# Kernel optimization log

Hardware: AMD Instinct MI355X
Metric: run time of the kernel (lower is better)

Reference implementation:

```python
import jax, jax.numpy as jnp
import numpy as np

B, D, DEPTH, C = 8192, 2048, 10, 1000
NUM_INNER = 2 ** DEPTH - 1   # 1023
NUM_LEAVES = 2 ** DEPTH      # 1024


def setup_inputs() -> dict:
    key = jax.random.key(0)
    k1, k2, k3, k4 = jax.random.split(key, 4)
    x = jax.random.normal(k1, (B, D), dtype=jnp.float32)
    # scale weights like a typical init so sigmoid isn't fully saturated
    W = jax.random.normal(k2, (D, NUM_INNER), dtype=jnp.float32) * 0.02
    b = jax.random.normal(k3, (NUM_INNER,), dtype=jnp.float32) * 0.02
    leaf_dist = jax.random.normal(k4, (NUM_LEAVES, C), dtype=jnp.float32)
    return {"x": x, "W": W, "b": b, "leaf_dist": leaf_dist}


def reference(x, W, b, leaf_dist):
    # inner node routing probabilities: [B, num_inner]
    decisions = jax.nn.sigmoid(x @ W + b)
    depth = int(np.log2(decisions.shape[1] + 1))
    pp = jnp.ones((x.shape[0], 1), dtype=x.dtype)  # path probs, starts at root
    for d in range(depth):  # small fixed loop over tree depth
        s, e = 2 ** d - 1, 2 ** (d + 1) - 1
        ld = decisions[:, s:e]                      # [B, 2^d]
        pp = jnp.concatenate([pp * ld, pp * (1.0 - ld)], axis=1)  # [B, 2^(d+1)]
        # faithful reproduction of the original's even/odd reordering
        pp = jnp.concatenate([pp[:, ::2], pp[:, 1::2]], axis=1)
    leaf_probs = jax.nn.softmax(leaf_dist, axis=1)  # [num_leaves, C]
    return pp @ leaf_probs                          # [B, C]
```

## Files before the change

kernel.cpp:

```cpp
#include <hip/hip_runtime.h>

typedef __attribute__((ext_vector_type(8))) unsigned short ushort8v;
typedef __attribute__((ext_vector_type(8))) __bf16 bf16x8;
typedef __attribute__((ext_vector_type(4))) float floatx4;

__device__ __forceinline__ unsigned short f2b(float f) {
    unsigned u = __float_as_uint(f);
    unsigned r = u + 0x7fffu + ((u >> 16) & 1u);
    return (unsigned short)(r >> 16);
}
__device__ __forceinline__ float b2f(unsigned short h) {
    return __uint_as_float(((unsigned)h) << 16);
}

__device__ __forceinline__ void gload16(const void* g, void* l) {
    __builtin_amdgcn_global_load_lds(
        (const __attribute__((address_space(1))) unsigned int*)g,
        (__attribute__((address_space(3))) unsigned int*)l,
        16, 0, 0);
}


__global__ __launch_bounds__(256) void prep_kernel(const float* __restrict__ x,
                                                   unsigned short* __restrict__ A2x,
                                                   const float* __restrict__ W,
                                                   unsigned short* __restrict__ B2w,
                                                   const float* __restrict__ ld_,
                                                   unsigned short* __restrict__ B2p) {
    __shared__ float tile[32 * 33];
    __shared__ float buf[1000];
    __shared__ float red[8];
    const int b = blockIdx.x, t = threadIdx.x;
    if (b < 2048) {
        const int mt = b >> 2, kq = (b & 3) * 64;
        const int kco = t >> 4, l16 = t & 15;
        const float* xr0 = x + (size_t)(mt * 16 + l16) * 2048;
#pragma unroll
        for (int i = 0; i < 4; i++) {
            const int kc = kq + i * 16 + kco;
            const float* xr = xr0 + kc * 8;
            float4 v0 = *(const float4*)xr;
            float4 v1 = *(const float4*)(xr + 4);
            ushort8v o;
            o[0] = f2b(v0.x); o[1] = f2b(v0.y); o[2] = f2b(v0.z); o[3] = f2b(v0.w);
            o[4] = f2b(v1.x); o[5] = f2b(v1.y); o[6] = f2b(v1.z); o[7] = f2b(v1.w);
            *(ushort8v*)(A2x + ((size_t)(mt * 256 + kc) * 16 + l16) * 8) = o;
        }
    } else if (b < 4096) {
        const int idx = b - 2048;
        const int n0 = (idx & 31) * 32, k0 = (idx >> 5) * 32;
        const int tx = t & 31, ty = t >> 5;
#pragma unroll
        for (int i = 0; i < 4; i++) {
            int k = k0 + ty + i * 8, n = n0 + tx;
            tile[(ty + i * 8) * 33 + tx] = (n < 1023) ? W[(size_t)k * 1023 + n] : 0.f;
        }
        __syncthreads();
#pragma unroll
        for (int i = 0; i < 4; i++) {
            int n = n0 + ty + i * 8, k = k0 + tx;
            size_t off = ((size_t)((n >> 4) * 256 + (k >> 3)) * 16 + (n & 15)) * 8 + (k & 7);
            B2w[off] = f2b(tile[tx * 33 + ty + i * 8]);
        }
    } else {
        const int l0 = b - 4096;
        const float* r = ld_ + (size_t)l0 * 1000;
        float mx = -3.4e38f;
        for (int i = t; i < 1000; i += 256) { float v = r[i]; buf[i] = v; mx = fmaxf(mx, v); }
#pragma unroll
        for (int o = 32; o > 0; o >>= 1) mx = fmaxf(mx, __shfl_down(mx, o));
        if ((t & 63) == 0) red[t >> 6] = mx;
        __syncthreads();
        mx = fmaxf(fmaxf(red[0], red[1]), fmaxf(red[2], red[3]));
        float s = 0.f;
        for (int i = t; i < 1000; i += 256) { float e = __expf(buf[i] - mx); buf[i] = e; s += e; }
#pragma unroll
        for (int o = 32; o > 0; o >>= 1) s += __shfl_down(s, o);
        if ((t & 63) == 0) red[4 + (t >> 6)] = s;
        __syncthreads();
        float inv = 1.f / (red[4] + red[5] + red[6] + red[7]);
        for (int i = t; i < 1024; i += 256) {
            float pv = (i < 1000) ? buf[i] * inv : 0.f;
            size_t off = ((size_t)((i >> 4) * 128 + (l0 >> 3)) * 16 + (i & 15)) * 8 + (l0 & 7);
            B2p[off] = f2b(pv);
        }
    }
}

__global__ __launch_bounds__(256) void pp_kernel(const unsigned short* __restrict__ dec,
                                                 unsigned short* __restrict__ A2p) {
    __shared__ unsigned short dsh[8 * 1024];
    __shared__ float pa[8 * 1024];
    __shared__ float pb[8 * 1024];
    const int t = threadIdx.x;
    const int r0 = blockIdx.x * 8;
    {
        const ushort8v* src = (const ushort8v*)(dec + (size_t)r0 * 1024);
        ushort8v* dst = (ushort8v*)dsh;
        for (int g = t; g < 1024; g += 256) dst[g] = src[g];
    }
    if (t < 8) pa[t * 1024] = 1.f;
    __syncthreads();
    float* cur = pa; float* nxt = pb;
    for (int dep = 0; dep < 10; dep++) {
        const int half = 1 << dep;
        const int len  = half << 1;
        const int total = len << 3;
        for (int idx = t; idx < total; idx += 256) {
            const int r = idx >> (dep + 1);
            const int j = idx & (len - 1);
            int tt = j >> dep;
            int s  = j & (half - 1);
            int i2 = 2 * s + tt;
            int u  = i2 >> dep;
            int rr = i2 & (half - 1);
            float dv = b2f(dsh[r * 1024 + half - 1 + rr]);
            nxt[r * 1024 + j] = cur[r * 1024 + rr] * (u ? (1.f - dv) : dv);
        }
        __syncthreads();
        float* tmp = cur; cur = nxt; nxt = tmp;
    }
    for (int i = t; i < 8192; i += 256) {
        const int r = i >> 10, j = i & 1023;
        const int rrow = r0 + r;
        size_t off = ((size_t)((rrow >> 4) * 128 + (j >> 3)) * 16 + (rrow & 15)) * 8 + (j & 7);
        A2p[off] = f2b(cur[r * 1024 + j]);
    }
}

#define VMW(N) asm volatile("s_waitcnt vmcnt(" #N ")" ::: "memory")

#define M1_STEP(ks_, CUR_, STG_, VM_, DOSTAGE_)                                       \
    {                                                                                 \
        if (DOSTAGE_) STAGE((ks_) + 2, (STG_));                                       \
        VMW(VM_);                                                                     \
        __builtin_amdgcn_s_barrier();                                                 \
        const unsigned short* lA = &lds[(CUR_)][0];                                   \
        const unsigned short* lB = &lds[(CUR_)][8192];                                \
        bf16x8 af[4], bv[4];                                                          \
        _Pragma("unroll")                                                             \
        for (int m2 = 0; m2 < 4; m2++)                                                \
            af[m2] = __builtin_bit_cast(bf16x8,                                       \
                *(const ushort8v*)&lA[((wr * 4 + m2) * 4 + quad) * 128 + l16 * 8]);   \
        _Pragma("unroll")                                                             \
        for (int n2 = 0; n2 < 4; n2++)                                                \
            bv[n2] = __builtin_bit_cast(bf16x8,                                       \
                *(const ushort8v*)&lB[((wc * 4 + n2) * 4 + quad) * 128 + l16 * 8]);   \
        asm volatile("s_waitcnt lgkmcnt(0)" ::: "memory");                            \
        __builtin_amdgcn_sched_barrier(0);                                            \
        __builtin_amdgcn_s_setprio(1);                                                \
        _Pragma("unroll")                                                             \
        for (int m2 = 0; m2 < 4; m2++)                                                \
            _Pragma("unroll")                                                         \
            for (int n2 = 0; n2 < 4; n2++)                                            \
                acc[m2][n2] = __builtin_amdgcn_mfma_f32_16x16x32_bf16(                \
                    af[m2], bv[n2], acc[m2][n2], 0, 0, 0);                            \
        __builtin_amdgcn_s_setprio(0);                                                \
        __builtin_amdgcn_s_barrier();                                                 \
    }

__global__ __launch_bounds__(512, 1) void gemm_m1(const unsigned short* __restrict__ A2,
                                                  const unsigned short* __restrict__ B2,
                                                  const float* __restrict__ bias,
                                                  unsigned short* __restrict__ obf) {
    constexpr int KC = 256;
    __shared__ unsigned short lds[3][12288];

    const int tid  = threadIdx.x;
    const int lane = tid & 63;
    const int wave = tid >> 6;
    const int quad = lane >> 4, l16 = lane & 15;
    const int wr = wave >> 1, wc = wave & 1;

    const int bid = blockIdx.x;
    const int xcd = bid & 7;
    const int j   = bid >> 3;
    const int bm  = xcd * 4 + (j & 3);
    const int bn  = j >> 2;

    const int cA  = tid >> 4;
    const int sub = (tid & 15) * 8;
    const unsigned short* gA0 = A2 + ((size_t)(bm * 16 + (cA >> 2))        * KC + (cA & 3)) * 128 + sub;
    const unsigned short* gA1 = A2 + ((size_t)(bm * 16 + ((cA + 32) >> 2)) * KC + (cA & 3)) * 128 + sub;
    const unsigned short* gB0 = B2 + ((size_t)(bn * 8  + (cA >> 2))        * KC + (cA & 3)) * 128 + sub;
    const int dA0 = cA * 128 + sub;
    const int dA1 = (cA + 32) * 128 + sub;
    const int dB0 = 8192 + cA * 128 + sub;

    floatx4 acc[4][4] = {};
    constexpr int nks = KC / 4;

    auto STAGE = [&](int ks, int b) {
        const size_t ko = (size_t)ks * 512;
        gload16(gA0 + ko, &lds[b][dA0]);
        gload16(gA1 + ko, &lds[b][dA1]);
        gload16(gB0 + ko, &lds[b][dB0]);
    };

    STAGE(0, 0); STAGE(1, 1);

    int c0 = 0, c1 = 1, c2 = 2;
    for (int ks = 0; ks < nks - 2; ++ks) {
        M1_STEP(ks, c0, c2, 6, true);
        int tmp = c0; c0 = c1; c1 = c2; c2 = tmp;
    }
    M1_STEP(nks - 2, c0, c2, 3, false);
    { int tmp = c0; c0 = c1; c1 = c2; c2 = tmp; }
    M1_STEP(nks - 1, c0, c2, 0, false);

    const int mt0 = bm * 16 + wr * 4;
    const int nt0 = bn * 8  + wc * 4;
#pragma unroll
    for (int n2 = 0; n2 < 4; n2++) {
        const int col = (nt0 + n2) * 16 + l16;
        const float bbias = (col < 1023) ? bias[col] : 0.f;
#pragma unroll
        for (int m2 = 0; m2 < 4; m2++) {
            const int row0 = (mt0 + m2) * 16 + quad * 4;
#pragma unroll
            for (int r = 0; r < 4; r++) {
                float sgm = 1.f / (1.f + __expf(-(acc[m2][n2][r] + bbias)));
                obf[(size_t)(row0 + r) * 1024 + col] = f2b(sgm);
            }
        }
    }
}

#define P4_STEP(ks_, b_, VM_, DOSTAGE_)                                             \
    {                                                                               \
        VMW(VM_);                                                                   \
        __builtin_amdgcn_s_barrier();                                               \
        __builtin_amdgcn_sched_barrier(0);                                          \
        const unsigned short* lA = &lds[(b_)][0];                                   \
        const unsigned short* lB = &lds[(b_)][4096];                                \
        bf16x8 af[4], bv[4];                                                        \
        _Pragma("unroll")                                                           \
        for (int m2 = 0; m2 < 4; m2++)                                              \
            af[m2] = __builtin_bit_cast(bf16x8,                                     \
                *(const ushort8v*)&lA[((wr * 4 + m2) * 4 + quad) * 128 + l16 * 8]); \
        _Pragma("unroll")                                                           \
        for (int n2 = 0; n2 < 4; n2++)                                              \
            bv[n2] = __builtin_bit_cast(bf16x8,                                     \
                *(const ushort8v*)&lB[((wc * 4 + n2) * 4 + quad) * 128 + l16 * 8]); \
        asm volatile("s_waitcnt lgkmcnt(0)" ::: "memory");                          \
        __builtin_amdgcn_sched_barrier(0);                                          \
        __builtin_amdgcn_s_barrier();                                               \
        __builtin_amdgcn_sched_barrier(0);                                          \
        if (DOSTAGE_) STAGE((ks_) + 4, (b_));                                       \
        __builtin_amdgcn_s_setprio(1);                                              \
        _Pragma("unroll")                                                           \
        for (int m2 = 0; m2 < 4; m2++)                                              \
            _Pragma("unroll")                                                       \
            for (int n2 = 0; n2 < 4; n2++)                                          \
                acc[m2][n2] = __builtin_amdgcn_mfma_f32_16x16x32_bf16(              \
                    af[m2], bv[n2], acc[m2][n2], 0, 0, 0);                          \
        __builtin_amdgcn_s_setprio(0);                                              \
    }

template <int KC>
__global__ __launch_bounds__(256, 2) void gemm_p4(const unsigned short* __restrict__ A2,
                                                  const unsigned short* __restrict__ B2,
                                                  float* __restrict__ of32, int ldo) {
    __shared__ unsigned short lds[4][8192];

    const int tid  = threadIdx.x;
    const int lane = tid & 63;
    const int wave = tid >> 6;
    const int quad = lane >> 4, l16 = lane & 15;
    const int wr = wave >> 1, wc = wave & 1;

    const int bid = blockIdx.x;
    const int xcd = bid & 7;
    const int j   = bid >> 3;
    const int bm  = xcd * 8 + (j & 7);
    const int bn  = j >> 3;

    const int c0  = tid >> 4;
    const int sub = (tid & 15) * 8;
    const unsigned short* gA0 = A2 + ((size_t)(bm * 8 + (c0 >> 2))        * KC + (c0 & 3)) * 128 + sub;
    const unsigned short* gA1 = A2 + ((size_t)(bm * 8 + ((c0 + 16) >> 2)) * KC + (c0 & 3)) * 128 + sub;
    const unsigned short* gB0 = B2 + ((size_t)(bn * 8 + (c0 >> 2))        * KC + (c0 & 3)) * 128 + sub;
    const unsigned short* gB1 = B2 + ((size_t)(bn * 8 + ((c0 + 16) >> 2)) * KC + (c0 & 3)) * 128 + sub;
    const int dA0 = c0 * 128 + sub;
    const int dA1 = (c0 + 16) * 128 + sub;
    const int dB0 = 4096 + c0 * 128 + sub;
    const int dB1 = 4096 + (c0 + 16) * 128 + sub;

    floatx4 acc[4][4] = {};
    constexpr int nks = KC / 4;

    auto STAGE = [&](int ks, int b) {
        const size_t ko = (size_t)ks * 512;
        gload16(gA0 + ko, &lds[b][dA0]);
        gload16(gA1 + ko, &lds[b][dA1]);
        gload16(gB0 + ko, &lds[b][dB0]);
        gload16(gB1 + ko, &lds[b][dB1]);
    };

    STAGE(0, 0); STAGE(1, 1); STAGE(2, 2); STAGE(3, 3);

    for (int ks = 0; ks < nks - 4; ++ks) {
        P4_STEP(ks, ks & 3, 12, true);
    }
    P4_STEP(nks - 4, (nks - 4) & 3, 12, false);
    P4_STEP(nks - 3, (nks - 3) & 3, 8,  false);
    P4_STEP(nks - 2, (nks - 2) & 3, 4,  false);
    P4_STEP(nks - 1, (nks - 1) & 3, 0,  false);

    const int mt0 = bm * 8 + wr * 4;
    const int nt0 = bn * 8 + wc * 4;
#pragma unroll
    for (int n2 = 0; n2 < 4; n2++) {
        const int col = (nt0 + n2) * 16 + l16;
#pragma unroll
        for (int m2 = 0; m2 < 4; m2++) {
            const int row0 = (mt0 + m2) * 16 + quad * 4;
#pragma unroll
            for (int r = 0; r < 4; r++) {
                if (col < 1000) of32[(size_t)(row0 + r) * ldo + col] = acc[m2][n2][r];
            }
        }
    }
}

extern "C" void kernel_launch(void* const* d_in, const int* in_sizes, int n_in,
                              void* d_out, int out_size, void* d_ws, size_t ws_size,
                              hipStream_t stream) {
    const float* x   = (const float*)d_in[0];
    const float* W   = (const float*)d_in[1];
    const float* b   = (const float*)d_in[2];
    const float* ldd = (const float*)d_in[3];
    float* out = (float*)d_out;

    char* ws = (char*)d_ws;
    unsigned short* A2x = (unsigned short*)(ws);
    unsigned short* A2p = (unsigned short*)(ws);
    unsigned short* B2w = (unsigned short*)(ws + 33554432);
    unsigned short* dec = (unsigned short*)(ws + 37748736);
    unsigned short* B2p = (unsigned short*)(ws + 54525952);

    prep_kernel<<<5120, 256, 0, stream>>>(x, A2x, W, B2w, ldd, B2p);
    gemm_m1<<<256, 512, 0, stream>>>(A2x, B2w, b, dec);
    pp_kernel<<<1024, 256, 0, stream>>>(dec, A2p);
    gemm_p4<128><<<512, 256, 0, stream>>>(A2p, B2p, out, 1000);
}
```

Baseline: 199.8 us.

## Vectorize prep/pp stores and compute first six tree levels directly

The x-conversion path now has each thread read a contiguous run of one row, and the W transpose writes 4 bf16 values per store instead of scalar stores. In pp_kernel, the first six tree levels are computed in closed form per leaf, as a product of six factors, instead of six barrier-separated passes. The iterative loop now starts at depth 6. The final A2p writeout uses 8-byte vector stores, cutting the count of scalar global stores and barriers at the cost of slightly more per-thread index math.

```diff
diff --git a/kernel.cpp b/kernel.cpp
--- a/kernel.cpp
+++ b/kernel.cpp
@@ -1,6 +1,7 @@
 #include <hip/hip_runtime.h>
 
 typedef __attribute__((ext_vector_type(8))) unsigned short ushort8v;
+typedef __attribute__((ext_vector_type(4))) unsigned short ushort4v;
 typedef __attribute__((ext_vector_type(8))) __bf16 bf16x8;
 typedef __attribute__((ext_vector_type(4))) float floatx4;
 
@@ -33,17 +34,17 @@
     const int b = blockIdx.x, t = threadIdx.x;
     if (b < 2048) {
         const int mt = b >> 2, kq = (b & 3) * 64;
-        const int kco = t >> 4, l16 = t & 15;
-        const float* xr0 = x + (size_t)(mt * 16 + l16) * 2048;
-#pragma unroll
-        for (int i = 0; i < 4; i++) {
-            const int kc = kq + i * 16 + kco;
-            const float* xr = xr0 + kc * 8;
-            float4 v0 = *(const float4*)xr;
-            float4 v1 = *(const float4*)(xr + 4);
+        const int l16 = t >> 4;
+        const int sg  = t & 15;
+        const float* xr = x + (size_t)(mt * 16 + l16) * 2048 + (size_t)(kq + sg * 4) * 8;
+#pragma unroll
+        for (int c = 0; c < 4; c++) {
+            float4 v0 = *(const float4*)(xr + c * 8);
+            float4 v1 = *(const float4*)(xr + c * 8 + 4);
             ushort8v o;
             o[0] = f2b(v0.x); o[1] = f2b(v0.y); o[2] = f2b(v0.z); o[3] = f2b(v0.w);
             o[4] = f2b(v1.x); o[5] = f2b(v1.y); o[6] = f2b(v1.z); o[7] = f2b(v1.w);
+            const int kc = kq + sg * 4 + c;
             *(ushort8v*)(A2x + ((size_t)(mt * 256 + kc) * 16 + l16) * 8) = o;
         }
     } else if (b < 4096) {
@@ -56,11 +57,15 @@
             tile[(ty + i * 8) * 33 + tx] = (n < 1023) ? W[(size_t)k * 1023 + n] : 0.f;
         }
         __syncthreads();
-#pragma unroll
-        for (int i = 0; i < 4; i++) {
-            int n = n0 + ty + i * 8, k = k0 + tx;
+        {
+            const int tx2 = t & 31, ky = t >> 5;
+            const int n = n0 + tx2;
+            const int k = k0 + ky * 4;
+            ushort4v o;
+#pragma unroll
+            for (int e = 0; e < 4; e++) o[e] = f2b(tile[(ky * 4 + e) * 33 + tx2]);
             size_t off = ((size_t)((n >> 4) * 256 + (k >> 3)) * 16 + (n & 15)) * 8 + (k & 7);
-            B2w[off] = f2b(tile[tx * 33 + ty + i * 8]);
+            *(ushort4v*)(B2w + off) = o;
         }
     } else {
         const int l0 = b - 4096;
@@ -99,10 +104,36 @@
         ushort8v* dst = (ushort8v*)dsh;
         for (int g = t; g < 1024; g += 256) dst[g] = src[g];
     }
-    if (t < 8) pa[t * 1024] = 1.f;
+    __syncthreads();
+    {
+        const int r  = t >> 5;
+        const int jb = (t & 31) * 2;
+        const unsigned short* dr = &dsh[r * 1024];
+#pragma unroll
+        for (int e = 0; e < 2; e++) {
+            int idx = jb + e;
+            float fac[6];
+#pragma unroll
+            for (int dep = 5; dep >= 0; --dep) {
+                const int half = 1 << dep;
+                const int tt = idx >> dep;
+                const int s  = idx & (half - 1);
+                const int i2 = 2 * s + tt;
+                const int u  = i2 >> dep;
+                const int rr = i2 & (half - 1);
+                const float dv = b2f(dr[half - 1 + rr]);
+                fac[dep] = u ? (1.f - dv) : dv;
+                idx = rr;
+            }
+            float prod = fac[0];
+#pragma unroll
+            for (int dep = 1; dep < 6; dep++) prod *= fac[dep];
+            pa[r * 1024 + jb + e] = prod;
+        }
+    }
     __syncthreads();
     float* cur = pa; float* nxt = pb;
-    for (int dep = 0; dep < 10; dep++) {
+    for (int dep = 6; dep < 10; dep++) {
         const int half = 1 << dep;
         const int len  = half << 1;
         const int total = len << 3;
@@ -120,11 +151,21 @@
         __syncthreads();
         float* tmp = cur; cur = nxt; nxt = tmp;
     }
-    for (int i = t; i < 8192; i += 256) {
-        const int r = i >> 10, j = i & 1023;
+    {
+        const int r  = t >> 5;
+        const int jb = (t & 31) * 32;
         const int rrow = r0 + r;
-        size_t off = ((size_t)((rrow >> 4) * 128 + (j >> 3)) * 16 + (rrow & 15)) * 8 + (j & 7);
-        A2p[off] = f2b(cur[r * 1024 + j]);
+        const float* cr = &cur[r * 1024];
+        const size_t rbase = (size_t)(rrow >> 4) * 128 * 128 + (size_t)(rrow & 15) * 8;
+#pragma unroll
+        for (int g = 0; g < 8; g++) {
+            const int j = jb + g * 4;
+            ushort4v o;
+            o[0] = f2b(cr[j]); o[1] = f2b(cr[j + 1]);
+            o[2] = f2b(cr[j + 2]); o[3] = f2b(cr[j + 3]);
+            size_t off = rbase + (size_t)(j >> 3) * 128 + (j & 7);
+            *(ushort4v*)(A2p + off) = o;
+        }
     }
 }
 
```

Result: no change. 198.7 us (-0.5%).

## Fuse prep, both GEMMs and path-prob stage into one cooperative persistent kernel

Applied to the files above, without the earlier changes.

Replaces the four separate launches (prep, decision GEMM, path-probability, output GEMM) with a single cooperative kernel of 256 blocks × 512 threads, separated by grid-wide syncs. The path-probability stage now computes each leaf's probability directly as a product of ten ancestor factors per thread, instead of level-by-level passes with block barriers. The W transpose also writes 4-wide vector stores. The aim is to remove inter-kernel launch gaps and the barrier-heavy tree expansion. The costs are grid.sync overhead, fixed one-block-per-CU occupancy, and redundant factor recomputation per leaf.

```diff
diff --git a/kernel.cpp b/kernel.cpp
--- a/kernel.cpp
+++ b/kernel.cpp
@@ -1,6 +1,10 @@
 #include <hip/hip_runtime.h>
+#include <hip/hip_cooperative_groups.h>
+
+namespace cg = cooperative_groups;
 
 typedef __attribute__((ext_vector_type(8))) unsigned short ushort8v;
+typedef __attribute__((ext_vector_type(4))) unsigned short ushort4v;
 typedef __attribute__((ext_vector_type(8))) __bf16 bf16x8;
 typedef __attribute__((ext_vector_type(4))) float floatx4;
 
@@ -12,7 +16,6 @@
 __device__ __forceinline__ float b2f(unsigned short h) {
     return __uint_as_float(((unsigned)h) << 16);
 }
-
 __device__ __forceinline__ void gload16(const void* g, void* l) {
     __builtin_amdgcn_global_load_lds(
         (const __attribute__((address_space(1))) unsigned int*)g,
@@ -20,123 +23,16 @@
         16, 0, 0);
 }
 
-
-__global__ __launch_bounds__(256) void prep_kernel(const float* __restrict__ x,
-                                                   unsigned short* __restrict__ A2x,
-                                                   const float* __restrict__ W,
-                                                   unsigned short* __restrict__ B2w,
-                                                   const float* __restrict__ ld_,
-                                                   unsigned short* __restrict__ B2p) {
-    __shared__ float tile[32 * 33];
-    __shared__ float buf[1000];
-    __shared__ float red[8];
-    const int b = blockIdx.x, t = threadIdx.x;
-    if (b < 2048) {
-        const int mt = b >> 2, kq = (b & 3) * 64;
-        const int kco = t >> 4, l16 = t & 15;
-        const float* xr0 = x + (size_t)(mt * 16 + l16) * 2048;
-#pragma unroll
-        for (int i = 0; i < 4; i++) {
-            const int kc = kq + i * 16 + kco;
-            const float* xr = xr0 + kc * 8;
-            float4 v0 = *(const float4*)xr;
-            float4 v1 = *(const float4*)(xr + 4);
-            ushort8v o;
-            o[0] = f2b(v0.x); o[1] = f2b(v0.y); o[2] = f2b(v0.z); o[3] = f2b(v0.w);
-            o[4] = f2b(v1.x); o[5] = f2b(v1.y); o[6] = f2b(v1.z); o[7] = f2b(v1.w);
-            *(ushort8v*)(A2x + ((size_t)(mt * 256 + kc) * 16 + l16) * 8) = o;
-        }
-    } else if (b < 4096) {
-        const int idx = b - 2048;
-        const int n0 = (idx & 31) * 32, k0 = (idx >> 5) * 32;
-        const int tx = t & 31, ty = t >> 5;
-#pragma unroll
-        for (int i = 0; i < 4; i++) {
-            int k = k0 + ty + i * 8, n = n0 + tx;
-            tile[(ty + i * 8) * 33 + tx] = (n < 1023) ? W[(size_t)k * 1023 + n] : 0.f;
-        }
-        __syncthreads();
-#pragma unroll
-        for (int i = 0; i < 4; i++) {
-            int n = n0 + ty + i * 8, k = k0 + tx;
-            size_t off = ((size_t)((n >> 4) * 256 + (k >> 3)) * 16 + (n & 15)) * 8 + (k & 7);
-            B2w[off] = f2b(tile[tx * 33 + ty + i * 8]);
-        }
-    } else {
-        const int l0 = b - 4096;
-        const float* r = ld_ + (size_t)l0 * 1000;
-        float mx = -3.4e38f;
-        for (int i = t; i < 1000; i += 256) { float v = r[i]; buf[i] = v; mx = fmaxf(mx, v); }
-#pragma unroll
-        for (int o = 32; o > 0; o >>= 1) mx = fmaxf(mx, __shfl_down(mx, o));
-        if ((t & 63) == 0) red[t >> 6] = mx;
-        __syncthreads();
-        mx = fmaxf(fmaxf(red[0], red[1]), fmaxf(red[2], red[3]));
-        float s = 0.f;
-        for (int i = t; i < 1000; i += 256) { float e = __expf(buf[i] - mx); buf[i] = e; s += e; }
-#pragma unroll
-        for (int o = 32; o > 0; o >>= 1) s += __shfl_down(s, o);
-        if ((t & 63) == 0) red[4 + (t >> 6)] = s;
-        __syncthreads();
-        float inv = 1.f / (red[4] + red[5] + red[6] + red[7]);
-        for (int i = t; i < 1024; i += 256) {
-            float pv = (i < 1000) ? buf[i] * inv : 0.f;
-            size_t off = ((size_t)((i >> 4) * 128 + (l0 >> 3)) * 16 + (i & 15)) * 8 + (l0 & 7);
-            B2p[off] = f2b(pv);
-        }
-    }
-}
-
-__global__ __launch_bounds__(256) void pp_kernel(const unsigned short* __restrict__ dec,
-                                                 unsigned short* __restrict__ A2p) {
-    __shared__ unsigned short dsh[8 * 1024];
-    __shared__ float pa[8 * 1024];
-    __shared__ float pb[8 * 1024];
-    const int t = threadIdx.x;
-    const int r0 = blockIdx.x * 8;
-    {
-        const ushort8v* src = (const ushort8v*)(dec + (size_t)r0 * 1024);
-        ushort8v* dst = (ushort8v*)dsh;
-        for (int g = t; g < 1024; g += 256) dst[g] = src[g];
-    }
-    if (t < 8) pa[t * 1024] = 1.f;
-    __syncthreads();
-    float* cur = pa; float* nxt = pb;
-    for (int dep = 0; dep < 10; dep++) {
-        const int half = 1 << dep;
-        const int len  = half << 1;
-        const int total = len << 3;
-        for (int idx = t; idx < total; idx += 256) {
-            const int r = idx >> (dep + 1);
-            const int j = idx & (len - 1);
-            int tt = j >> dep;
-            int s  = j & (half - 1);
-            int i2 = 2 * s + tt;
-            int u  = i2 >> dep;
-            int rr = i2 & (half - 1);
-            float dv = b2f(dsh[r * 1024 + half - 1 + rr]);
-            nxt[r * 1024 + j] = cur[r * 1024 + rr] * (u ? (1.f - dv) : dv);
-        }
-        __syncthreads();
-        float* tmp = cur; cur = nxt; nxt = tmp;
-    }
-    for (int i = t; i < 8192; i += 256) {
-        const int r = i >> 10, j = i & 1023;
-        const int rrow = r0 + r;
-        size_t off = ((size_t)((rrow >> 4) * 128 + (j >> 3)) * 16 + (rrow & 15)) * 8 + (j & 7);
-        A2p[off] = f2b(cur[r * 1024 + j]);
-    }
-}
-
 #define VMW(N) asm volatile("s_waitcnt vmcnt(" #N ")" ::: "memory")
+
 
 #define M1_STEP(ks_, CUR_, STG_, VM_, DOSTAGE_)                                       \
     {                                                                                 \
         if (DOSTAGE_) STAGE((ks_) + 2, (STG_));                                       \
         VMW(VM_);                                                                     \
         __builtin_amdgcn_s_barrier();                                                 \
-        const unsigned short* lA = &lds[(CUR_)][0];                                   \
-        const unsigned short* lB = &lds[(CUR_)][8192];                                \
+        const unsigned short* lA = &lds1[(CUR_)][0];                                  \
+        const unsigned short* lB = &lds1[(CUR_)][8192];                               \
         bf16x8 af[4], bv[4];                                                          \
         _Pragma("unroll")                                                             \
         for (int m2 = 0; m2 < 4; m2++)                                                \
@@ -159,94 +55,27 @@
         __builtin_amdgcn_s_barrier();                                                 \
     }
 
-__global__ __launch_bounds__(512, 1) void gemm_m1(const unsigned short* __restrict__ A2,
-                                                  const unsigned short* __restrict__ B2,
-                                                  const float* __restrict__ bias,
-                                                  unsigned short* __restrict__ obf) {
-    constexpr int KC = 256;
-    __shared__ unsigned short lds[3][12288];
-
-    const int tid  = threadIdx.x;
-    const int lane = tid & 63;
-    const int wave = tid >> 6;
-    const int quad = lane >> 4, l16 = lane & 15;
-    const int wr = wave >> 1, wc = wave & 1;
-
-    const int bid = blockIdx.x;
-    const int xcd = bid & 7;
-    const int j   = bid >> 3;
-    const int bm  = xcd * 4 + (j & 3);
-    const int bn  = j >> 2;
-
-    const int cA  = tid >> 4;
-    const int sub = (tid & 15) * 8;
-    const unsigned short* gA0 = A2 + ((size_t)(bm * 16 + (cA >> 2))        * KC + (cA & 3)) * 128 + sub;
-    const unsigned short* gA1 = A2 + ((size_t)(bm * 16 + ((cA + 32) >> 2)) * KC + (cA & 3)) * 128 + sub;
-    const unsigned short* gB0 = B2 + ((size_t)(bn * 8  + (cA >> 2))        * KC + (cA & 3)) * 128 + sub;
-    const int dA0 = cA * 128 + sub;
-    const int dA1 = (cA + 32) * 128 + sub;
-    const int dB0 = 8192 + cA * 128 + sub;
-
-    floatx4 acc[4][4] = {};
-    constexpr int nks = KC / 4;
-
-    auto STAGE = [&](int ks, int b) {
-        const size_t ko = (size_t)ks * 512;
-        gload16(gA0 + ko, &lds[b][dA0]);
-        gload16(gA1 + ko, &lds[b][dA1]);
-        gload16(gB0 + ko, &lds[b][dB0]);
-    };
-
-    STAGE(0, 0); STAGE(1, 1);
-
-    int c0 = 0, c1 = 1, c2 = 2;
-    for (int ks = 0; ks < nks - 2; ++ks) {
-        M1_STEP(ks, c0, c2, 6, true);
-        int tmp = c0; c0 = c1; c1 = c2; c2 = tmp;
-    }
-    M1_STEP(nks - 2, c0, c2, 3, false);
-    { int tmp = c0; c0 = c1; c1 = c2; c2 = tmp; }
-    M1_STEP(nks - 1, c0, c2, 0, false);
-
-    const int mt0 = bm * 16 + wr * 4;
-    const int nt0 = bn * 8  + wc * 4;
-#pragma unroll
-    for (int n2 = 0; n2 < 4; n2++) {
-        const int col = (nt0 + n2) * 16 + l16;
-        const float bbias = (col < 1023) ? bias[col] : 0.f;
-#pragma unroll
-        for (int m2 = 0; m2 < 4; m2++) {
-            const int row0 = (mt0 + m2) * 16 + quad * 4;
-#pragma unroll
-            for (int r = 0; r < 4; r++) {
-                float sgm = 1.f / (1.f + __expf(-(acc[m2][n2][r] + bbias)));
-                obf[(size_t)(row0 + r) * 1024 + col] = f2b(sgm);
-            }
-        }
-    }
-}
-
-#define P4_STEP(ks_, b_, VM_, DOSTAGE_)                                             \
+#define G2_STEP(ks_, b_, VM_, DOSTAGE_)                                             \
     {                                                                               \
         VMW(VM_);                                                                   \
         __builtin_amdgcn_s_barrier();                                               \
         __builtin_amdgcn_sched_barrier(0);                                          \
-        const unsigned short* lA = &lds[(b_)][0];                                   \
-        const unsigned short* lB = &lds[(b_)][4096];                                \
+        const unsigned short* lA = ldsg + (b_) * 8192;                              \
+        const unsigned short* lB = lA + 4096;                                       \
         bf16x8 af[4], bv[4];                                                        \
         _Pragma("unroll")                                                           \
         for (int m2 = 0; m2 < 4; m2++)                                              \
             af[m2] = __builtin_bit_cast(bf16x8,                                     \
-                *(const ushort8v*)&lA[((wr * 4 + m2) * 4 + quad) * 128 + l16 * 8]); \
+                *(const ushort8v*)&lA[((wr2 * 4 + m2) * 4 + quad) * 128 + l16 * 8]);\
         _Pragma("unroll")                                                           \
         for (int n2 = 0; n2 < 4; n2++)                                              \
             bv[n2] = __builtin_bit_cast(bf16x8,                                     \
-                *(const ushort8v*)&lB[((wc * 4 + n2) * 4 + quad) * 128 + l16 * 8]); \
+                *(const ushort8v*)&lB[((wc2 * 4 + n2) * 4 + quad) * 128 + l16 * 8]);\
         asm volatile("s_waitcnt lgkmcnt(0)" ::: "memory");                          \
         __builtin_amdgcn_sched_barrier(0);                                          \
         __builtin_amdgcn_s_barrier();                                               \
         __builtin_amdgcn_sched_barrier(0);                                          \
-        if (DOSTAGE_) STAGE((ks_) + 4, (b_));                                       \
+        if (DOSTAGE_) STG2((ks_) + 4, (b_));                                        \
         __builtin_amdgcn_s_setprio(1);                                              \
         _Pragma("unroll")                                                           \
         for (int m2 = 0; m2 < 4; m2++)                                              \
@@ -257,67 +86,262 @@
         __builtin_amdgcn_s_setprio(0);                                              \
     }
 
-template <int KC>
-__global__ __launch_bounds__(256, 2) void gemm_p4(const unsigned short* __restrict__ A2,
-                                                  const unsigned short* __restrict__ B2,
-                                                  float* __restrict__ of32, int ldo) {
-    __shared__ unsigned short lds[4][8192];
-
-    const int tid  = threadIdx.x;
-    const int lane = tid & 63;
-    const int wave = tid >> 6;
+__global__ __launch_bounds__(512, 1) void mega(const float* __restrict__ x,
+                                               const float* __restrict__ W,
+                                               const float* __restrict__ bias,
+                                               const float* __restrict__ ldd,
+                                               float* __restrict__ out,
+                                               unsigned short* __restrict__ A2x,
+                                               unsigned short* __restrict__ B2w,
+                                               unsigned short* __restrict__ dec,
+                                               unsigned short* __restrict__ B2p,
+                                               unsigned short* __restrict__ A2p) {
+    __shared__ __align__(16) unsigned char smem[131072];
+    cg::grid_group grid = cg::this_grid();
+
+    const int t   = threadIdx.x;
+    const int bid = blockIdx.x;
+    const int lane = t & 63;
+    const int wave = t >> 6;
     const int quad = lane >> 4, l16 = lane & 15;
-    const int wr = wave >> 1, wc = wave & 1;
-
-    const int bid = blockIdx.x;
-    const int xcd = bid & 7;
-    const int j   = bid >> 3;
-    const int bm  = xcd * 8 + (j & 7);
-    const int bn  = j >> 3;
-
-    const int c0  = tid >> 4;
-    const int sub = (tid & 15) * 8;
-    const unsigned short* gA0 = A2 + ((size_t)(bm * 8 + (c0 >> 2))        * KC + (c0 & 3)) * 128 + sub;
-    const unsigned short* gA1 = A2 + ((size_t)(bm * 8 + ((c0 + 16) >> 2)) * KC + (c0 & 3)) * 128 + sub;
-    const unsigned short* gB0 = B2 + ((size_t)(bn * 8 + (c0 >> 2))        * KC + (c0 & 3)) * 128 + sub;
-    const unsigned short* gB1 = B2 + ((size_t)(bn * 8 + ((c0 + 16) >> 2)) * KC + (c0 & 3)) * 128 + sub;
-    const int dA0 = c0 * 128 + sub;
-    const int dA1 = (c0 + 16) * 128 + sub;
-    const int dB0 = 4096 + c0 * 128 + sub;
-    const int dB1 = 4096 + (c0 + 16) * 128 + sub;
-
-    floatx4 acc[4][4] = {};
-    constexpr int nks = KC / 4;
-
-    auto STAGE = [&](int ks, int b) {
-        const size_t ko = (size_t)ks * 512;
-        gload16(gA0 + ko, &lds[b][dA0]);
-        gload16(gA1 + ko, &lds[b][dA1]);
-        gload16(gB0 + ko, &lds[b][dB0]);
-        gload16(gB1 + ko, &lds[b][dB1]);
-    };
-
-    STAGE(0, 0); STAGE(1, 1); STAGE(2, 2); STAGE(3, 3);
-
-    for (int ks = 0; ks < nks - 4; ++ks) {
-        P4_STEP(ks, ks & 3, 12, true);
-    }
-    P4_STEP(nks - 4, (nks - 4) & 3, 12, false);
-    P4_STEP(nks - 3, (nks - 3) & 3, 8,  false);
-    P4_STEP(nks - 2, (nks - 2) & 3, 4,  false);
-    P4_STEP(nks - 1, (nks - 1) & 3, 0,  false);
-
-    const int mt0 = bm * 8 + wr * 4;
-    const int nt0 = bn * 8 + wc * 4;
-#pragma unroll
-    for (int n2 = 0; n2 < 4; n2++) {
-        const int col = (nt0 + n2) * 16 + l16;
-#pragma unroll
-        for (int m2 = 0; m2 < 4; m2++) {
-            const int row0 = (mt0 + m2) * 16 + quad * 4;
-#pragma unroll
-            for (int r = 0; r < 4; r++) {
-                if (col < 1000) of32[(size_t)(row0 + r) * ldo + col] = acc[m2][n2][r];
+
+    {
+        const int xl16 = t & 15, kcol = t >> 4;
+        for (int uu = 0; uu < 4; uu++) {
+            const int u  = bid * 4 + uu;
+            const int mt = u >> 1, h = u & 1;
+            const float* xr0 = x + (size_t)(mt * 16 + xl16) * 2048;
+#pragma unroll
+            for (int i = 0; i < 4; i++) {
+                const int kc = h * 128 + i * 32 + kcol;
+                const float* xr = xr0 + kc * 8;
+                float4 v0 = *(const float4*)xr;
+                float4 v1 = *(const float4*)(xr + 4);
+                ushort8v o;
+                o[0] = f2b(v0.x); o[1] = f2b(v0.y); o[2] = f2b(v0.z); o[3] = f2b(v0.w);
+                o[4] = f2b(v1.x); o[5] = f2b(v1.y); o[6] = f2b(v1.z); o[7] = f2b(v1.w);
+                *(ushort8v*)(A2x + ((size_t)(mt * 256 + kc) * 16 + xl16) * 8) = o;
+            }
+        }
+    }
+    {
+        const int sub = t >> 8, tt = t & 255;
+        float* tl = (float*)smem + sub * (32 * 33);
+        const int tx = tt & 31, ty = tt >> 5;
+        for (int it = 0; it < 4; it++) {
+            const int idx = bid * 8 + it * 2 + sub;
+            const int n0 = (idx & 31) * 32, k0 = (idx >> 5) * 32;
+            __syncthreads();
+#pragma unroll
+            for (int i = 0; i < 4; i++) {
+                int k = k0 + ty + i * 8, n = n0 + tx;
+                tl[(ty + i * 8) * 33 + tx] = (n < 1023) ? W[(size_t)k * 1023 + n] : 0.f;
+            }
+            __syncthreads();
+            {
+                const int n = n0 + tx;
+                const int k = k0 + ty * 4;
+                ushort4v o;
+#pragma unroll
+                for (int e = 0; e < 4; e++) o[e] = f2b(tl[(ty * 4 + e) * 33 + tx]);
+                size_t off = ((size_t)((n >> 4) * 256 + (k >> 3)) * 16 + (n & 15)) * 8 + (k & 7);
+                *(ushort4v*)(B2w + off) = o;
+            }
+        }
+    }
+    {
+        const int sub = t >> 8, tt = t & 255;
+        float* bf = (float*)smem + sub * 1024;
+        float* rd = (float*)smem + 2048 + sub * 8;
+        for (int it = 0; it < 2; it++) {
+            const int l0 = bid * 4 + it * 2 + sub;
+            const float* r = ldd + (size_t)l0 * 1000;
+            __syncthreads();
+            float mx = -3.4e38f;
+            for (int i = tt; i < 1000; i += 256) { float v = r[i]; bf[i] = v; mx = fmaxf(mx, v); }
+#pragma unroll
+            for (int o = 32; o > 0; o >>= 1) mx = fmaxf(mx, __shfl_down(mx, o));
+            if ((tt & 63) == 0) rd[tt >> 6] = mx;
+            __syncthreads();
+            mx = fmaxf(fmaxf(rd[0], rd[1]), fmaxf(rd[2], rd[3]));
+            float s = 0.f;
+            for (int i = tt; i < 1000; i += 256) { float e = __expf(bf[i] - mx); bf[i] = e; s += e; }
+#pragma unroll
+            for (int o = 32; o > 0; o >>= 1) s += __shfl_down(s, o);
+            if ((tt & 63) == 0) rd[4 + (tt >> 6)] = s;
+            __syncthreads();
+            float inv = 1.f / (rd[4] + rd[5] + rd[6] + rd[7]);
+            for (int i = tt; i < 1024; i += 256) {
+                float pv = (i < 1000) ? bf[i] * inv : 0.f;
+                size_t off = ((size_t)((i >> 4) * 128 + (l0 >> 3)) * 16 + (i & 15)) * 8 + (l0 & 7);
+                B2p[off] = f2b(pv);
+            }
+        }
+    }
+    grid.sync();
+
+    {
+        constexpr int KC = 256;
+        unsigned short (*lds1)[12288] = (unsigned short(*)[12288])smem;
+
+        const int wr = wave >> 1, wc = wave & 1;
+
+        const int xcd = bid & 7;
+        const int j   = bid >> 3;
+        const int bm  = xcd * 4 + (j & 3);
+        const int bn  = j >> 2;
+
+        const int cA  = t >> 4;
+        const int sub = (t & 15) * 8;
+        const unsigned short* gA0 = A2x + ((size_t)(bm * 16 + (cA >> 2))        * KC + (cA & 3)) * 128 + sub;
+        const unsigned short* gA1 = A2x + ((size_t)(bm * 16 + ((cA + 32) >> 2)) * KC + (cA & 3)) * 128 + sub;
+        const unsigned short* gB0 = B2w + ((size_t)(bn * 8  + (cA >> 2))        * KC + (cA & 3)) * 128 + sub;
+        const int dA0 = cA * 128 + sub;
+        const int dA1 = (cA + 32) * 128 + sub;
+        const int dB0 = 8192 + cA * 128 + sub;
+
+        floatx4 acc[4][4] = {};
+        constexpr int nks = KC / 4;
+
+        auto STAGE = [&](int ks, int b) {
+            const size_t ko = (size_t)ks * 512;
+            gload16(gA0 + ko, &lds1[b][dA0]);
+            gload16(gA1 + ko, &lds1[b][dA1]);
+            gload16(gB0 + ko, &lds1[b][dB0]);
+        };
+
+        STAGE(0, 0); STAGE(1, 1);
+        int c0 = 0, c1 = 1, c2 = 2;
+        for (int ks = 0; ks < nks - 2; ++ks) {
+            M1_STEP(ks, c0, c2, 6, true);
+            int tmp = c0; c0 = c1; c1 = c2; c2 = tmp;
+        }
+        M1_STEP(nks - 2, c0, c2, 3, false);
+        { int tmp = c0; c0 = c1; c1 = c2; c2 = tmp; }
+        M1_STEP(nks - 1, c0, c2, 0, false);
+
+        const int mt0 = bm * 16 + wr * 4;
+        const int nt0 = bn * 8  + wc * 4;
+#pragma unroll
+        for (int n2 = 0; n2 < 4; n2++) {
+            const int col = (nt0 + n2) * 16 + l16;
+            const float bbias = (col < 1023) ? bias[col] : 0.f;
+#pragma unroll
+            for (int m2 = 0; m2 < 4; m2++) {
+                const int row0 = (mt0 + m2) * 16 + quad * 4;
+#pragma unroll
+                for (int r = 0; r < 4; r++) {
+                    float sgm = 1.f / (1.f + __expf(-(acc[m2][n2][r] + bbias)));
+                    dec[(size_t)(row0 + r) * 1024 + col] = f2b(sgm);
+                }
+            }
+        }
+    }
+    grid.sync();
+
+    {
+        const int sub = t >> 8, tt = t & 255;
+        unsigned short* ds = (unsigned short*)smem + sub * 16384;
+        const int unit = bid * 2 + sub;
+        __syncthreads();
+        {
+            const ushort8v* src = (const ushort8v*)(dec + (size_t)unit * 16 * 1024);
+            ushort8v* dst = (ushort8v*)ds;
+            for (int g = tt; g < 2048; g += 256) dst[g] = src[g];
+        }
+        __syncthreads();
+        const int r = tt & 15;
+        const unsigned short* dr = ds + r * 1024;
+        const size_t rbase = (size_t)unit * 16384 + (size_t)r * 8;
+#pragma unroll
+        for (int g2 = 0; g2 < 8; g2++) {
+            const int jb = (tt >> 4) * 8 + g2 * 128;
+            ushort8v o;
+#pragma unroll
+            for (int e = 0; e < 8; e++) {
+                int idx = jb + e;
+                float fac[10];
+#pragma unroll
+                for (int dep = 9; dep >= 0; --dep) {
+                    const int half = 1 << dep;
+                    const int tb = idx >> dep;
+                    const int s  = idx & (half - 1);
+                    const int i2 = 2 * s + tb;
+                    const int u2 = i2 >> dep;
+                    const int rr = i2 & (half - 1);
+                    const float dv = b2f(dr[half - 1 + rr]);
+                    fac[dep] = u2 ? (1.f - dv) : dv;
+                    idx = rr;
+                }
+                float prod = fac[0];
+#pragma unroll
+                for (int dep = 1; dep < 10; dep++) prod *= fac[dep];
+                o[e] = f2b(prod);
+            }
+            *(ushort8v*)(A2p + rbase + (size_t)(jb >> 3) * 128) = o;
+        }
+    }
+    grid.sync();
+
+    {
+        constexpr int KC = 128;
+        const int g4   = wave >> 2;
+        const int tid4 = t & 255;
+        const int wv4  = wave & 3;
+        const int wr2 = wv4 >> 1, wc2 = wv4 & 1;
+        unsigned short* ldsg = (unsigned short*)smem + g4 * 32768;
+
+        const int bid2 = bid * 2 + g4;
+        const int xcd = bid2 & 7;
+        const int j   = bid2 >> 3;
+        const int bm  = xcd * 8 + (j & 7);
+        const int bn  = j >> 3;
+
+        const int c02 = tid4 >> 4;
+        const int sb  = (tid4 & 15) * 8;
+        const unsigned short* gA0w = A2p + ((size_t)(bm * 8 + (c02 >> 2))        * KC + (c02 & 3)) * 128 + sb;
+        const unsigned short* gA1w = A2p + ((size_t)(bm * 8 + ((c02 + 16) >> 2)) * KC + (c02 & 3)) * 128 + sb;
+        const unsigned short* gB0w = B2p + ((size_t)(bn * 8 + (c02 >> 2))        * KC + (c02 & 3)) * 128 + sb;
+        const unsigned short* gB1w = B2p + ((size_t)(bn * 8 + ((c02 + 16) >> 2)) * KC + (c02 & 3)) * 128 + sb;
+        const int dA0w = c02 * 128 + sb;
+        const int dA1w = (c02 + 16) * 128 + sb;
+        const int dB0w = 4096 + c02 * 128 + sb;
+        const int dB1w = 4096 + (c02 + 16) * 128 + sb;
+
+        floatx4 acc[4][4] = {};
+        constexpr int nks = KC / 4;
+
+        auto STG2 = [&](int ks, int b) {
+            const size_t ko = (size_t)ks * 512;
+            unsigned short* lb = ldsg + b * 8192;
+            gload16(gA0w + ko, lb + dA0w);
+            gload16(gA1w + ko, lb + dA1w);
+            gload16(gB0w + ko, lb + dB0w);
+            gload16(gB1w + ko, lb + dB1w);
+        };
+
+        STG2(0, 0); STG2(1, 1); STG2(2, 2); STG2(3, 3);
+
+        for (int ks = 0; ks < nks - 4; ++ks) {
+            G2_STEP(ks, ks & 3, 12, true);
+        }
+        G2_STEP(nks - 4, (nks - 4) & 3, 12, false);
+        G2_STEP(nks - 3, (nks - 3) & 3, 8,  false);
+        G2_STEP(nks - 2, (nks - 2) & 3, 4,  false);
+        G2_STEP(nks - 1, (nks - 1) & 3, 0,  false);
+
+        const int mt0 = bm * 8 + wr2 * 4;
+        const int nt0 = bn * 8 + wc2 * 4;
+#pragma unroll
+        for (int n2 = 0; n2 < 4; n2++) {
+            const int col = (nt0 + n2) * 16 + l16;
+#pragma unroll
+            for (int m2 = 0; m2 < 4; m2++) {
+                const int row0 = (mt0 + m2) * 16 + quad * 4;
+#pragma unroll
+                for (int r = 0; r < 4; r++) {
+                    if (col < 1000) out[(size_t)(row0 + r) * 1000 + col] = acc[m2][n2][r];
+                }
             }
         }
     }
@@ -339,8 +363,7 @@
     unsigned short* dec = (unsigned short*)(ws + 37748736);
     unsigned short* B2p = (unsigned short*)(ws + 54525952);
 
-    prep_kernel<<<5120, 256, 0, stream>>>(x, A2x, W, B2w, ldd, B2p);
-    gemm_m1<<<256, 512, 0, stream>>>(A2x, B2w, b, dec);
-    pp_kernel<<<1024, 256, 0, stream>>>(dec, A2p);
-    gemm_p4<128><<<512, 256, 0, stream>>>(A2p, B2p, out, 1000);
-}
+    void* args[] = {(void*)&x, (void*)&W, (void*)&b, (void*)&ldd, (void*)&out,
+                    (void*)&A2x, (void*)&B2w, (void*)&dec, (void*)&B2p, (void*)&A2p};
+    hipLaunchCooperativeKernel((const void*)mega, dim3(256), dim3(512), args, 0, stream);
+}
```

New measurement: 373.5 us. 1.87x slower.
